# Performance work log

Measured on AMD Instinct MI355X. Metric: run time of the kernel, lower is better.

## Reference

```python
import jax, jax.numpy as jnp
import numpy as np

N = 100000
E = 1600000
IN, HID, OUT = 128, 64, 32


def setup_inputs() -> dict:
    key = jax.random.key(0)
    k1, k2, k3, k4, k5, k6 = jax.random.split(key, 6)
    x = jax.random.normal(k1, (N, IN), dtype=jnp.float32)
    edge_index = jax.random.randint(k2, (2, E), 0, N, dtype=jnp.int64)
    # Glorot-style init for the two GCNConv layers (weight + bias each)
    W1 = jax.random.normal(k3, (IN, HID), dtype=jnp.float32) / np.sqrt(IN)
    b1 = jnp.zeros((HID,), dtype=jnp.float32)
    W2 = jax.random.normal(k4, (HID, OUT), dtype=jnp.float32) / np.sqrt(HID)
    b2 = jnp.zeros((OUT,), dtype=jnp.float32)
    return {"x": x, "edge_index": edge_index, "W1": W1, "b1": b1, "W2": W2, "b2": b2}


def _gcn_norm(edge_index, n, dtype):
    """Add self-loops and compute symmetric normalization coefficients.
    Returns (row, col, norm) where norm[e] = deg[row]^-1/2 * deg[col]^-1/2."""
    loops = jnp.tile(jnp.arange(n, dtype=edge_index.dtype)[None, :], (2, 1))
    ei = jnp.concatenate([edge_index, loops], axis=1)  # [2, E+N]
    row, col = ei[0], ei[1]
    deg = jax.ops.segment_sum(jnp.ones(col.shape, dtype), col, num_segments=n)
    dinv = jnp.where(deg > 0, jax.lax.rsqrt(deg), 0.0)
    norm = dinv[row] * dinv[col]
    return row, col, norm


def _gcn_conv(h, W, b, row, col, norm, n):
    h = h @ W                                   # [N, F_out] dense transform first
    msg = h[row] * norm[:, None]                # gather + edge-normalize
    out = jax.ops.segment_sum(msg, col, num_segments=n)  # scatter-add
    return out + b


def reference(x, edge_index, W1, b1, W2, b2):
    n = x.shape[0]
    row, col, norm = _gcn_norm(edge_index, n, x.dtype)
    h = jax.nn.relu(_gcn_conv(x, W1, b1, row, col, norm, n))
    return _gcn_conv(h, W2, b2, row, col, norm, n)
```

## Files before the change

### kernel.cpp

```cpp
#include <hip/hip_runtime.h>


#define CDIV(a, b) (((a) + (b)-1) / (b))
#define EDGE_TILE 8192
#define BUCKET_CAP 4608

__device__ inline unsigned short f2bf(float f) {
    unsigned int u = __float_as_uint(f);
    u += 0x7FFF + ((u >> 16) & 1);
    return (unsigned short)(u >> 16);
}
__device__ inline void bf2x2(unsigned int u, float& lo, float& hi) {
    lo = __uint_as_float(u << 16);
    hi = __uint_as_float(u & 0xFFFF0000u);
}

__global__ __launch_bounds__(256, 3) void k_sort_gemm1(
    const int* __restrict__ row, const int* __restrict__ col, int e,
    int* __restrict__ gcur, int* __restrict__ bucket,
    const float* __restrict__ x, const float* __restrict__ W,
    unsigned short* __restrict__ hb, int n, int nb_sort) {
    __shared__ float4 smem4[2560];
    int t = threadIdx.x;
    if ((int)blockIdx.x < nb_sort) {
        int* ints   = (int*)smem4;
        int* hist   = ints;
        int* lstart = ints + 512;
        int* rbase  = ints + 1024;
        int* lcur   = ints + 1536;
        int* ent    = ints + 2048;
        int base = blockIdx.x * EDGE_TILE;
        int cnt = min(EDGE_TILE, e - base);
        int nbuck = (n + 255) >> 8;
        hist[t] = 0; hist[t + 256] = 0;
        __syncthreads();
        for (int i = t; i < cnt; i += 256) atomicAdd(&hist[col[base + i] >> 8], 1);
        __syncthreads();
        int h0 = hist[2 * t], h1 = hist[2 * t + 1];
        int sum2 = h0 + h1;
        lcur[t] = sum2;
        __syncthreads();
        for (int d = 1; d < 256; d <<= 1) {
            int v = (t >= d) ? lcur[t - d] : 0;
            __syncthreads();
            lcur[t] += v;
            __syncthreads();
        }
        int excl2 = lcur[t] - sum2;
        lstart[2 * t] = excl2;
        lstart[2 * t + 1] = excl2 + h0;
        __syncthreads();
        for (int b = t; b < 512; b += 256) {
            int hbv = hist[b];
            rbase[b] = (hbv > 0) ? atomicAdd(&gcur[b], hbv) : 0;
            lcur[b] = 0;
        }
        __syncthreads();
        for (int i = t; i < cnt; i += 256) {
            int c = col[base + i], r = row[base + i];
            int b = c >> 8;
            int rk = atomicAdd(&lcur[b], 1);
            ent[lstart[b] + rk] = ((c & 255) << 17) | r;
        }
        __syncthreads();
        for (int i = t; i < cnt; i += 256) {
            int lo = 0, hi = nbuck - 1;
            while (lo < hi) {
                int mid = (lo + hi + 1) >> 1;
                if (lstart[mid] <= i) lo = mid; else hi = mid - 1;
            }
            int b = lo;
            int gi = rbase[b] + (i - lstart[b]);
            if (gi < BUCKET_CAP) bucket[(size_t)b * BUCKET_CAP + gi] = ent[i];
        }
    } else {
        float4* xs = smem4;
        int base = ((int)blockIdx.x - nb_sort) * 64;
        int nodes = min(64, n - base);
        const float4* xg = (const float4*)(x + (size_t)base * 128);
        int lim = nodes * 32;
#pragma unroll
        for (int i = 0; i < 8; ++i) {
            int idx = t + i * 256;
            if (idx < lim) xs[idx] = xg[idx];
        }
        __syncthreads();
        int j = t & 63, g = t >> 6;
        float acc[16];
#pragma unroll
        for (int mm = 0; mm < 16; ++mm) acc[mm] = 0.f;
#pragma unroll 8
        for (int k4 = 0; k4 < 32; ++k4) {
            float w0 = W[(k4 * 4 + 0) * 64 + j];
            float w1 = W[(k4 * 4 + 1) * 64 + j];
            float w2 = W[(k4 * 4 + 2) * 64 + j];
            float w3 = W[(k4 * 4 + 3) * 64 + j];
#pragma unroll
            for (int mm = 0; mm < 16; ++mm) {
                float4 xv = xs[(mm * 4 + g) * 32 + k4];
                acc[mm] = fmaf(xv.x, w0, acc[mm]);
                acc[mm] = fmaf(xv.y, w1, acc[mm]);
                acc[mm] = fmaf(xv.z, w2, acc[mm]);
                acc[mm] = fmaf(xv.w, w3, acc[mm]);
            }
        }
#pragma unroll
        for (int mm = 0; mm < 16; ++mm) {
            int m = base + mm * 4 + g;
            if (m < n) hb[(size_t)m * 64 + j] = f2bf(acc[mm]);
        }
    }
}

__global__ __launch_bounds__(512) void k_bscan(const int* __restrict__ gcur,
                                               int* __restrict__ gbase, int nb) {
    __shared__ int s[512];
    int t = threadIdx.x;
    int v = (t < nb) ? min(gcur[t], BUCKET_CAP) : 0;
    s[t] = v;
    __syncthreads();
    for (int d = 1; d < 512; d <<= 1) {
        int a = (t >= d) ? s[t - d] : 0;
        __syncthreads();
        s[t] += a;
        __syncthreads();
    }
    if (t < nb) gbase[t] = s[t] - v;
}

__global__ __launch_bounds__(256) void k_csr(
    const int* __restrict__ gcur, const int* __restrict__ gbase,
    const int* __restrict__ bucket, int* __restrict__ csr,
    int* __restrict__ start, int* __restrict__ cntg, float* __restrict__ dinv,
    int n) {
    __shared__ int hist[256], lstart[256], lcur[256];
    __shared__ int csrbuf[BUCKET_CAP];
    int b = blockIdx.x, t = threadIdx.x;
    int nodebase = b << 8;
    int nnode = min(256, n - nodebase);
    int m = min(gcur[b], BUCKET_CAP);
    const int* ent = bucket + (size_t)b * BUCKET_CAP;
    hist[t] = 0;
    __syncthreads();
    for (int i = t; i < m; i += 256) atomicAdd(&hist[ent[i] >> 17], 1);
    __syncthreads();
    int v = hist[t];
    lstart[t] = v;
    __syncthreads();
    for (int d = 1; d < 256; d <<= 1) {
        int a = (t >= d) ? lstart[t - d] : 0;
        __syncthreads();
        lstart[t] += a;
        __syncthreads();
    }
    int excl = lstart[t] - v;
    int gb = gbase[b];
    if (t < nnode) {
        int node = nodebase + t;
        start[node] = gb + excl;
        cntg[node] = v;
        dinv[node] = rsqrtf((float)(v + 1));
    }
    __syncthreads();
    lstart[t] = excl;
    lcur[t] = 0;
    __syncthreads();
    for (int i = t; i < m; i += 256) {
        int en = ent[i];
        int local = en >> 17;
        int rk = atomicAdd(&lcur[local], 1);
        csrbuf[lstart[local] + rk] = en & 0x1FFFF;
    }
    __syncthreads();
    for (int i = t; i < m; i += 256) csr[gb + i] = csrbuf[i];
}

__global__ __launch_bounds__(256) void k_agg1(const int* __restrict__ start,
                                              const int* __restrict__ cnt,
                                              const int* __restrict__ csr,
                                              const float* __restrict__ dinv,
                                              const unsigned short* __restrict__ hbm,
                                              const float* __restrict__ b,
                                              float* __restrict__ out, int n) {
    int node = (blockIdx.x * 256 + threadIdx.x) >> 6;
    if (node >= n) return;
    int lane = threadIdx.x & 63;
    int q = lane >> 3;
    int f4 = lane & 7;
    const int* cs = csr + start[node];
    int d = cnt[node];
    const uint4* hb = (const uint4*)hbm;
    float a0[8], a1[8];
#pragma unroll
    for (int k = 0; k < 8; ++k) { a0[k] = 0.f; a1[k] = 0.f; }
    int j = q;
    for (; j + 8 < d; j += 16) {
        int r0 = cs[j], r1 = cs[j + 8];
        float d0 = dinv[r0], d1 = dinv[r1];
        uint4 v0 = hb[(size_t)r0 * 8 + f4];
        uint4 v1 = hb[(size_t)r1 * 8 + f4];
        float lo, hi;
        bf2x2(v0.x, lo, hi); a0[0] = fmaf(lo, d0, a0[0]); a0[1] = fmaf(hi, d0, a0[1]);
        bf2x2(v0.y, lo, hi); a0[2] = fmaf(lo, d0, a0[2]); a0[3] = fmaf(hi, d0, a0[3]);
        bf2x2(v0.z, lo, hi); a0[4] = fmaf(lo, d0, a0[4]); a0[5] = fmaf(hi, d0, a0[5]);
        bf2x2(v0.w, lo, hi); a0[6] = fmaf(lo, d0, a0[6]); a0[7] = fmaf(hi, d0, a0[7]);
        bf2x2(v1.x, lo, hi); a1[0] = fmaf(lo, d1, a1[0]); a1[1] = fmaf(hi, d1, a1[1]);
        bf2x2(v1.y, lo, hi); a1[2] = fmaf(lo, d1, a1[2]); a1[3] = fmaf(hi, d1, a1[3]);
        bf2x2(v1.z, lo, hi); a1[4] = fmaf(lo, d1, a1[4]); a1[5] = fmaf(hi, d1, a1[5]);
        bf2x2(v1.w, lo, hi); a1[6] = fmaf(lo, d1, a1[6]); a1[7] = fmaf(hi, d1, a1[7]);
    }
    if (j < d) {
        int r = cs[j];
        float d0 = dinv[r];
        uint4 v0 = hb[(size_t)r * 8 + f4];
        float lo, hi;
        bf2x2(v0.x, lo, hi); a0[0] = fmaf(lo, d0, a0[0]); a0[1] = fmaf(hi, d0, a0[1]);
        bf2x2(v0.y, lo, hi); a0[2] = fmaf(lo, d0, a0[2]); a0[3] = fmaf(hi, d0, a0[3]);
        bf2x2(v0.z, lo, hi); a0[4] = fmaf(lo, d0, a0[4]); a0[5] = fmaf(hi, d0, a0[5]);
        bf2x2(v0.w, lo, hi); a0[6] = fmaf(lo, d0, a0[6]); a0[7] = fmaf(hi, d0, a0[7]);
    }
#pragma unroll
    for (int k = 0; k < 8; ++k) a0[k] += a1[k];
#pragma unroll
    for (int k = 0; k < 8; ++k) {
        a0[k] += __shfl_xor(a0[k], 8, 64);
        a0[k] += __shfl_xor(a0[k], 16, 64);
        a0[k] += __shfl_xor(a0[k], 32, 64);
    }
    if (q == 0) {
        float dc = dinv[node];
        uint4 sv = hb[(size_t)node * 8 + f4];
        float s[8], lo, hi;
        bf2x2(sv.x, lo, hi); s[0] = lo; s[1] = hi;
        bf2x2(sv.y, lo, hi); s[2] = lo; s[3] = hi;
        bf2x2(sv.z, lo, hi); s[4] = lo; s[5] = hi;
        bf2x2(sv.w, lo, hi); s[6] = lo; s[7] = hi;
        const float4* b4 = (const float4*)b;
        float4 bv0 = b4[f4 * 2], bv1 = b4[f4 * 2 + 1];
        float4 o0, o1;
        o0.x = fmaxf(fmaf(s[0], dc, a0[0]) * dc + bv0.x, 0.f);
        o0.y = fmaxf(fmaf(s[1], dc, a0[1]) * dc + bv0.y, 0.f);
        o0.z = fmaxf(fmaf(s[2], dc, a0[2]) * dc + bv0.z, 0.f);
        o0.w = fmaxf(fmaf(s[3], dc, a0[3]) * dc + bv0.w, 0.f);
        o1.x = fmaxf(fmaf(s[4], dc, a0[4]) * dc + bv1.x, 0.f);
        o1.y = fmaxf(fmaf(s[5], dc, a0[5]) * dc + bv1.y, 0.f);
        o1.z = fmaxf(fmaf(s[6], dc, a0[6]) * dc + bv1.z, 0.f);
        o1.w = fmaxf(fmaf(s[7], dc, a0[7]) * dc + bv1.w, 0.f);
        float4* o4 = (float4*)out;
        o4[(size_t)node * 16 + f4 * 2]     = o0;
        o4[(size_t)node * 16 + f4 * 2 + 1] = o1;
    }
}

__global__ __launch_bounds__(256) void k_gemm2(const float* __restrict__ a,
                                               const float* __restrict__ W,
                                               const float* __restrict__ dinv,
                                               unsigned short* __restrict__ hb, int n) {
    __shared__ float4 as[64 * 16];
    int base = blockIdx.x * 64;
    int t = threadIdx.x;
    int nodes = min(64, n - base);
    const float4* ag = (const float4*)(a + (size_t)base * 64);
    int lim = nodes * 16;
#pragma unroll
    for (int i = 0; i < 4; ++i) {
        int idx = t + i * 256;
        if (idx < lim) as[idx] = ag[idx];
    }
    __syncthreads();
    int j = t & 31, g = t >> 5;
    float acc[8];
#pragma unroll
    for (int mm = 0; mm < 8; ++mm) acc[mm] = 0.f;
#pragma unroll 8
    for (int k4 = 0; k4 < 16; ++k4) {
        float w0 = W[(k4 * 4 + 0) * 32 + j];
        float w1 = W[(k4 * 4 + 1) * 32 + j];
        float w2 = W[(k4 * 4 + 2) * 32 + j];
        float w3 = W[(k4 * 4 + 3) * 32 + j];
#pragma unroll
        for (int mm = 0; mm < 8; ++mm) {
            float4 xv = as[(mm * 8 + g) * 16 + k4];
            acc[mm] = fmaf(xv.x, w0, acc[mm]);
            acc[mm] = fmaf(xv.y, w1, acc[mm]);
            acc[mm] = fmaf(xv.z, w2, acc[mm]);
            acc[mm] = fmaf(xv.w, w3, acc[mm]);
        }
    }
#pragma unroll
    for (int mm = 0; mm < 8; ++mm) {
        int m = base + mm * 8 + g;
        if (m < n) hb[(size_t)m * 32 + j] = f2bf(acc[mm] * dinv[m]);
    }
}

__global__ __launch_bounds__(256) void k_agg2(const int* __restrict__ start,
                                              const int* __restrict__ cnt,
                                              const int* __restrict__ csr,
                                              const float* __restrict__ dinv,
                                              const unsigned short* __restrict__ hbm,
                                              const float* __restrict__ b,
                                              float* __restrict__ out, int n) {
    int node = (blockIdx.x * 256 + threadIdx.x) >> 6;
    if (node >= n) return;
    int lane = threadIdx.x & 63;
    int q = lane >> 2;
    int f4 = lane & 3;
    const int* cs = csr + start[node];
    int d = cnt[node];
    const uint4* hb = (const uint4*)hbm;
    float a0[8], a1[8];
#pragma unroll
    for (int k = 0; k < 8; ++k) { a0[k] = 0.f; a1[k] = 0.f; }
    int j = q;
    for (; j + 16 < d; j += 32) {
        int r0 = cs[j], r1 = cs[j + 16];
        uint4 v0 = hb[(size_t)r0 * 4 + f4];
        uint4 v1 = hb[(size_t)r1 * 4 + f4];
        float lo, hi;
        bf2x2(v0.x, lo, hi); a0[0] += lo; a0[1] += hi;
        bf2x2(v0.y, lo, hi); a0[2] += lo; a0[3] += hi;
        bf2x2(v0.z, lo, hi); a0[4] += lo; a0[5] += hi;
        bf2x2(v0.w, lo, hi); a0[6] += lo; a0[7] += hi;
        bf2x2(v1.x, lo, hi); a1[0] += lo; a1[1] += hi;
        bf2x2(v1.y, lo, hi); a1[2] += lo; a1[3] += hi;
        bf2x2(v1.z, lo, hi); a1[4] += lo; a1[5] += hi;
        bf2x2(v1.w, lo, hi); a1[6] += lo; a1[7] += hi;
    }
    if (j < d) {
        int r = cs[j];
        uint4 v0 = hb[(size_t)r * 4 + f4];
        float lo, hi;
        bf2x2(v0.x, lo, hi); a0[0] += lo; a0[1] += hi;
        bf2x2(v0.y, lo, hi); a0[2] += lo; a0[3] += hi;
        bf2x2(v0.z, lo, hi); a0[4] += lo; a0[5] += hi;
        bf2x2(v0.w, lo, hi); a0[6] += lo; a0[7] += hi;
    }
#pragma unroll
    for (int k = 0; k < 8; ++k) a0[k] += a1[k];
#pragma unroll
    for (int k = 0; k < 8; ++k) {
        a0[k] += __shfl_xor(a0[k], 4, 64);
        a0[k] += __shfl_xor(a0[k], 8, 64);
        a0[k] += __shfl_xor(a0[k], 16, 64);
        a0[k] += __shfl_xor(a0[k], 32, 64);
    }
    if (q == 0) {
        float dc = dinv[node];
        uint4 sv = hb[(size_t)node * 4 + f4];
        float s[8], lo, hi;
        bf2x2(sv.x, lo, hi); s[0] = lo; s[1] = hi;
        bf2x2(sv.y, lo, hi); s[2] = lo; s[3] = hi;
        bf2x2(sv.z, lo, hi); s[4] = lo; s[5] = hi;
        bf2x2(sv.w, lo, hi); s[6] = lo; s[7] = hi;
        const float4* b4 = (const float4*)b;
        float4 bv0 = b4[f4 * 2], bv1 = b4[f4 * 2 + 1];
        float4 o0, o1;
        o0.x = (a0[0] + s[0]) * dc + bv0.x;
        o0.y = (a0[1] + s[1]) * dc + bv0.y;
        o0.z = (a0[2] + s[2]) * dc + bv0.z;
        o0.w = (a0[3] + s[3]) * dc + bv0.w;
        o1.x = (a0[4] + s[4]) * dc + bv1.x;
        o1.y = (a0[5] + s[5]) * dc + bv1.y;
        o1.z = (a0[6] + s[6]) * dc + bv1.z;
        o1.w = (a0[7] + s[7]) * dc + bv1.w;
        float4* o4 = (float4*)out;
        o4[(size_t)node * 8 + f4 * 2]     = o0;
        o4[(size_t)node * 8 + f4 * 2 + 1] = o1;
    }
}

extern "C" void kernel_launch(void* const* d_in, const int* in_sizes, int n_in,
                              void* d_out, int out_size, void* d_ws, size_t ws_size,
                              hipStream_t stream) {
    const float* x  = (const float*)d_in[0];
    const int*   ei = (const int*)d_in[1];
    const float* W1 = (const float*)d_in[2];
    const float* b1 = (const float*)d_in[3];
    const float* W2 = (const float*)d_in[4];
    const float* b2 = (const float*)d_in[5];
    float* out = (float*)d_out;

    const int n = in_sizes[0] / 128;
    const int e = in_sizes[1] / 2;
    const int* rowp = ei;
    const int* colp = ei + e;

    const int nbuck = CDIV(n, 256);
    const int nb_sort = CDIV(e, EDGE_TILE);
    const int nb_gemm1 = CDIV(n, 64);

    int*   gcur  = (int*)d_ws;
    int*   gbase = gcur + 512;
    int*   start = gbase + 512;
    int*   cnt   = start + n;
    float* dinv  = (float*)(cnt + n);
    int*   csr   = (int*)(dinv + n);
    unsigned short* h1b = (unsigned short*)(csr + e);
    float* aggbuf = (float*)(h1b + (size_t)n * 64);
    int*   bucket = (int*)aggbuf;
    unsigned short* h2b = h1b;

    hipMemsetAsync(gcur, 0, 512 * sizeof(int), stream);

    k_sort_gemm1<<<nb_sort + nb_gemm1, 256, 0, stream>>>(
        rowp, colp, e, gcur, bucket, x, W1, h1b, n, nb_sort);
    k_bscan<<<1, 512, 0, stream>>>(gcur, gbase, nbuck);
    k_csr<<<nbuck, 256, 0, stream>>>(gcur, gbase, bucket, csr, start, cnt, dinv, n);

    k_agg1<<<CDIV(n * 64, 256), 256, 0, stream>>>(start, cnt, csr, dinv, h1b, b1, aggbuf, n);
    k_gemm2<<<CDIV(n, 64), 256, 0, stream>>>(aggbuf, W2, dinv, h2b, n);
    k_agg2<<<CDIV(n * 64, 256), 256, 0, stream>>>(start, cnt, csr, dinv, h2b, b2, out, n);
}
```

Measured before the change: 262.4 us.

## Fuse second-layer GEMM into first aggregation and shrink sort shared memory

The layer-2 dense transform (64→32, scaled by dinv, stored as bf16) now runs inside k_agg1. Each wave stages its ReLU'd row in shared memory and does a 32-wide dot product per lane against W2. This removes the separate k_gemm2 launch and the fp32 round trip of the intermediate aggregation buffer through global memory. Separately, the sort kernel reuses the histogram array as the local cursor, which cuts shared memory and raises launch bounds to 4 blocks per CU. The fused path drops the node<n early return, which relies on n being a multiple of 4. It also rereads W2 per wave instead of amortising it across 64 nodes.

```diff
diff --git a/kernel.cpp b/kernel.cpp
--- a/kernel.cpp
+++ b/kernel.cpp
@@ -15,20 +15,19 @@
     hi = __uint_as_float(u & 0xFFFF0000u);
 }
 
-__global__ __launch_bounds__(256, 3) void k_sort_gemm1(
+__global__ __launch_bounds__(256, 4) void k_sort_gemm1(
     const int* __restrict__ row, const int* __restrict__ col, int e,
     int* __restrict__ gcur, int* __restrict__ bucket,
     const float* __restrict__ x, const float* __restrict__ W,
     unsigned short* __restrict__ hb, int n, int nb_sort) {
-    __shared__ float4 smem4[2560];
+    __shared__ float4 smem4[2432];
     int t = threadIdx.x;
     if ((int)blockIdx.x < nb_sort) {
         int* ints   = (int*)smem4;
-        int* hist   = ints;
-        int* lstart = ints + 512;
-        int* rbase  = ints + 1024;
-        int* lcur   = ints + 1536;
-        int* ent    = ints + 2048;
+        int* lstart = ints;
+        int* rbase  = ints + 512;
+        int* hist   = ints + 1024;
+        int* ent    = ints + 1536;
         int base = blockIdx.x * EDGE_TILE;
         int cnt = min(EDGE_TILE, e - base);
         int nbuck = (n + 255) >> 8;
@@ -38,28 +37,28 @@
         __syncthreads();
         int h0 = hist[2 * t], h1 = hist[2 * t + 1];
         int sum2 = h0 + h1;
-        lcur[t] = sum2;
+        rbase[t] = sum2;
         __syncthreads();
         for (int d = 1; d < 256; d <<= 1) {
-            int v = (t >= d) ? lcur[t - d] : 0;
+            int v = (t >= d) ? rbase[t - d] : 0;
             __syncthreads();
-            lcur[t] += v;
+            rbase[t] += v;
             __syncthreads();
         }
-        int excl2 = lcur[t] - sum2;
+        int excl2 = rbase[t] - sum2;
+        __syncthreads();
         lstart[2 * t] = excl2;
         lstart[2 * t + 1] = excl2 + h0;
-        __syncthreads();
         for (int b = t; b < 512; b += 256) {
             int hbv = hist[b];
             rbase[b] = (hbv > 0) ? atomicAdd(&gcur[b], hbv) : 0;
-            lcur[b] = 0;
+            hist[b] = 0;
         }
         __syncthreads();
         for (int i = t; i < cnt; i += 256) {
             int c = col[base + i], r = row[base + i];
             int b = c >> 8;
-            int rk = atomicAdd(&lcur[b], 1);
+            int rk = atomicAdd(&hist[b], 1);
             ent[lstart[b] + rk] = ((c & 255) << 17) | r;
         }
         __syncthreads();
@@ -181,14 +180,17 @@
                                               const float* __restrict__ dinv,
                                               const unsigned short* __restrict__ hbm,
                                               const float* __restrict__ b,
-                                              float* __restrict__ out, int n) {
+                                              const float* __restrict__ W2,
+                                              unsigned short* __restrict__ h2b, int n) {
+    __shared__ float rowbuf[4][64];
     int node = (blockIdx.x * 256 + threadIdx.x) >> 6;
-    if (node >= n) return;
+    int w = threadIdx.x >> 6;
     int lane = threadIdx.x & 63;
     int q = lane >> 3;
     int f4 = lane & 7;
     const int* cs = csr + start[node];
     int d = cnt[node];
+    float dc = dinv[node];
     const uint4* hb = (const uint4*)hbm;
     float a0[8], a1[8];
 #pragma unroll
@@ -228,7 +230,6 @@
         a0[k] += __shfl_xor(a0[k], 32, 64);
     }
     if (q == 0) {
-        float dc = dinv[node];
         uint4 sv = hb[(size_t)node * 8 + f4];
         float s[8], lo, hi;
         bf2x2(sv.x, lo, hi); s[0] = lo; s[1] = hi;
@@ -237,61 +238,24 @@
         bf2x2(sv.w, lo, hi); s[6] = lo; s[7] = hi;
         const float4* b4 = (const float4*)b;
         float4 bv0 = b4[f4 * 2], bv1 = b4[f4 * 2 + 1];
-        float4 o0, o1;
-        o0.x = fmaxf(fmaf(s[0], dc, a0[0]) * dc + bv0.x, 0.f);
-        o0.y = fmaxf(fmaf(s[1], dc, a0[1]) * dc + bv0.y, 0.f);
-        o0.z = fmaxf(fmaf(s[2], dc, a0[2]) * dc + bv0.z, 0.f);
-        o0.w = fmaxf(fmaf(s[3], dc, a0[3]) * dc + bv0.w, 0.f);
-        o1.x = fmaxf(fmaf(s[4], dc, a0[4]) * dc + bv1.x, 0.f);
-        o1.y = fmaxf(fmaf(s[5], dc, a0[5]) * dc + bv1.y, 0.f);
-        o1.z = fmaxf(fmaf(s[6], dc, a0[6]) * dc + bv1.z, 0.f);
-        o1.w = fmaxf(fmaf(s[7], dc, a0[7]) * dc + bv1.w, 0.f);
-        float4* o4 = (float4*)out;
-        o4[(size_t)node * 16 + f4 * 2]     = o0;
-        o4[(size_t)node * 16 + f4 * 2 + 1] = o1;
-    }
-}
-
-__global__ __launch_bounds__(256) void k_gemm2(const float* __restrict__ a,
-                                               const float* __restrict__ W,
-                                               const float* __restrict__ dinv,
-                                               unsigned short* __restrict__ hb, int n) {
-    __shared__ float4 as[64 * 16];
-    int base = blockIdx.x * 64;
-    int t = threadIdx.x;
-    int nodes = min(64, n - base);
-    const float4* ag = (const float4*)(a + (size_t)base * 64);
-    int lim = nodes * 16;
-#pragma unroll
-    for (int i = 0; i < 4; ++i) {
-        int idx = t + i * 256;
-        if (idx < lim) as[idx] = ag[idx];
-    }
-    __syncthreads();
-    int j = t & 31, g = t >> 5;
-    float acc[8];
-#pragma unroll
-    for (int mm = 0; mm < 8; ++mm) acc[mm] = 0.f;
+        rowbuf[w][f4 * 8 + 0] = fmaxf(fmaf(s[0], dc, a0[0]) * dc + bv0.x, 0.f);
+        rowbuf[w][f4 * 8 + 1] = fmaxf(fmaf(s[1], dc, a0[1]) * dc + bv0.y, 0.f);
+        rowbuf[w][f4 * 8 + 2] = fmaxf(fmaf(s[2], dc, a0[2]) * dc + bv0.z, 0.f);
+        rowbuf[w][f4 * 8 + 3] = fmaxf(fmaf(s[3], dc, a0[3]) * dc + bv0.w, 0.f);
+        rowbuf[w][f4 * 8 + 4] = fmaxf(fmaf(s[4], dc, a0[4]) * dc + bv1.x, 0.f);
+        rowbuf[w][f4 * 8 + 5] = fmaxf(fmaf(s[5], dc, a0[5]) * dc + bv1.y, 0.f);
+        rowbuf[w][f4 * 8 + 6] = fmaxf(fmaf(s[6], dc, a0[6]) * dc + bv1.z, 0.f);
+        rowbuf[w][f4 * 8 + 7] = fmaxf(fmaf(s[7], dc, a0[7]) * dc + bv1.w, 0.f);
+    }
+    __syncthreads();
+    int jj = lane & 31, half = lane >> 5;
+    const float* rw = rowbuf[w] + half * 32;
+    const float* Wk = W2 + half * 32 * 32 + jj;
+    float acc = 0.f;
 #pragma unroll 8
-    for (int k4 = 0; k4 < 16; ++k4) {
-        float w0 = W[(k4 * 4 + 0) * 32 + j];
-        float w1 = W[(k4 * 4 + 1) * 32 + j];
-        float w2 = W[(k4 * 4 + 2) * 32 + j];
-        float w3 = W[(k4 * 4 + 3) * 32 + j];
-#pragma unroll
-        for (int mm = 0; mm < 8; ++mm) {
-            float4 xv = as[(mm * 8 + g) * 16 + k4];
-            acc[mm] = fmaf(xv.x, w0, acc[mm]);
-            acc[mm] = fmaf(xv.y, w1, acc[mm]);
-            acc[mm] = fmaf(xv.z, w2, acc[mm]);
-            acc[mm] = fmaf(xv.w, w3, acc[mm]);
-        }
-    }
-#pragma unroll
-    for (int mm = 0; mm < 8; ++mm) {
-        int m = base + mm * 8 + g;
-        if (m < n) hb[(size_t)m * 32 + j] = f2bf(acc[mm] * dinv[m]);
-    }
+    for (int k = 0; k < 32; ++k) acc = fmaf(rw[k], Wk[k * 32], acc);
+    acc += __shfl_xor(acc, 32, 64);
+    if (half == 0) h2b[(size_t)node * 32 + jj] = f2bf(acc * dc);
 }
 
 __global__ __launch_bounds__(256) void k_agg2(const int* __restrict__ start,
@@ -397,9 +361,8 @@
     float* dinv  = (float*)(cnt + n);
     int*   csr   = (int*)(dinv + n);
     unsigned short* h1b = (unsigned short*)(csr + e);
-    float* aggbuf = (float*)(h1b + (size_t)n * 64);
-    int*   bucket = (int*)aggbuf;
-    unsigned short* h2b = h1b;
+    int*   bucket = (int*)(h1b + (size_t)n * 64);
+    unsigned short* h2b = (unsigned short*)bucket;
 
     hipMemsetAsync(gcur, 0, 512 * sizeof(int), stream);
 
@@ -408,7 +371,6 @@
     k_bscan<<<1, 512, 0, stream>>>(gcur, gbase, nbuck);
     k_csr<<<nbuck, 256, 0, stream>>>(gcur, gbase, bucket, csr, start, cnt, dinv, n);
 
-    k_agg1<<<CDIV(n * 64, 256), 256, 0, stream>>>(start, cnt, csr, dinv, h1b, b1, aggbuf, n);
-    k_gemm2<<<CDIV(n, 64), 256, 0, stream>>>(aggbuf, W2, dinv, h2b, n);
+    k_agg1<<<CDIV(n * 64, 256), 256, 0, stream>>>(start, cnt, csr, dinv, h1b, b1, W2, h2b, n);
     k_agg2<<<CDIV(n * 64, 256), 256, 0, stream>>>(start, cnt, csr, dinv, h2b, b2, out, n);
 }
```

New measurement: 262.7 us. No clear change (+0.1%).
